# Kernel tuning notes

Hardware: AMD Instinct MI355X
Metric: run time of the kernel (lower is better)

## Reference

```python
import jax, jax.numpy as jnp
import numpy as np
import math

E, H, O, D, HD, NH, NQ, TIN = 1152, 1280, 2432, 4, 64, 20, 64, 320
FF = 4 * H
B, N = 32, 577


def _ln(x, g, b, eps=1e-5):
    m = jnp.mean(x, axis=-1, keepdims=True)
    v = jnp.var(x, axis=-1, keepdims=True)
    return (x - m) * jax.lax.rsqrt(v + eps) * g + b


def _time_proj(t):
    # get_timestep_embedding, flip_sin_to_cos=True, freq_shift=0 -> [cos, sin]
    half = TIN // 2
    freqs = jnp.exp(-math.log(10000.0) * jnp.arange(half, dtype=jnp.float32) / half)
    ang = t[:, None] * freqs[None, :]
    return jnp.concatenate([jnp.cos(ang), jnp.sin(ang)], axis=-1)


def setup_inputs() -> dict:
    key = jax.random.key(0)
    ks = iter(jax.random.split(key, 64))
    def w(shape, s=0.02):
        return jax.random.normal(next(ks), shape, jnp.float32) * s
    return {
        "x": jax.random.normal(next(ks), (B, N, E), jnp.float32),
        "timestep": jax.random.uniform(next(ks), (B,), jnp.float32) * 1000.0,
        "latents0": jax.random.normal(next(ks), (1, NQ, H), jnp.float32) / math.sqrt(H),
        "proj_in_W": w((E, H)), "proj_in_b": jnp.zeros((H,), jnp.float32),
        "te1_W": w((TIN, H)), "te1_b": jnp.zeros((H,), jnp.float32),
        "te2_W": w((H, H)), "te2_b": jnp.zeros((H,), jnp.float32),
        "ln0_g": jnp.ones((D, H), jnp.float32), "ln0_b": jnp.zeros((D, H), jnp.float32),
        "ln1_g": jnp.ones((D, H), jnp.float32), "ln1_b": jnp.zeros((D, H), jnp.float32),
        "Wq": w((D, H, H)), "Wkv": w((D, H, 2 * H)), "Wo": w((D, H, H)),
        "ada_W": w((D, H, 4 * H)), "ada_b": jnp.zeros((D, 4 * H), jnp.float32),
        "lnada_g": jnp.ones((D, H), jnp.float32), "lnada_b": jnp.zeros((D, H), jnp.float32),
        "Wff1": w((D, H, FF)), "Wff2": w((D, FF, H)),
        "proj_out_W": w((H, O)), "proj_out_b": jnp.zeros((O,), jnp.float32),
        "norm_out_g": jnp.ones((O,), jnp.float32), "norm_out_b": jnp.zeros((O,), jnp.float32),
    }


def _forward(x, timestep, latents0, proj_in_W, proj_in_b, te1_W, te1_b, te2_W, te2_b,
             ln0_g, ln0_b, ln1_g, ln1_b, Wq, Wkv, Wo, ada_W, ada_b, lnada_g, lnada_b,
             Wff1, Wff2, proj_out_W, proj_out_b, norm_out_g, norm_out_b):
    b = x.shape[0]
    t_emb = _time_proj(timestep)
    t_emb = jax.nn.silu(t_emb @ te1_W + te1_b) @ te2_W + te2_b  # [B,H]
    h = x @ proj_in_W + proj_in_b + t_emb[:, None]              # [B,N,H]
    lat = jnp.broadcast_to(latents0, (b, NQ, H))
    s = 1.0 / math.sqrt(math.sqrt(HD))
    for i in range(D):
        emb = jax.nn.silu(t_emb) @ ada_W[i] + ada_b[i]
        sh_msa, sc_msa, sh_mlp, sc_mlp = jnp.split(emb, 4, axis=1)
        res = lat
        xn = _ln(h, ln0_g[i], ln0_b[i])
        lm = _ln(lat, ln1_g[i], ln1_b[i]) * (1.0 + sc_msa[:, None]) + sh_msa[:, None]
        q = (lm @ Wq[i]).reshape(b, NQ, NH, HD).transpose(0, 2, 1, 3)
        kv = jnp.concatenate([xn, lm], axis=1) @ Wkv[i]         # [B,N+NQ,2H]
        k, v = jnp.split(kv, 2, axis=-1)
        nk = k.shape[1]
        k = k.reshape(b, nk, NH, HD).transpose(0, 2, 1, 3)
        v = v.reshape(b, nk, NH, HD).transpose(0, 2, 1, 3)
        wts = jnp.einsum('bhqd,bhkd->bhqk', q * s, k * s)
        wts = jax.nn.softmax(wts.astype(jnp.float32), axis=-1).astype(q.dtype)
        att = jnp.einsum('bhqk,bhkd->bhqd', wts, v).transpose(0, 2, 1, 3).reshape(b, NQ, H)
        lat = att @ Wo[i] + res
        res = lat
        lm2 = _ln(lat, lnada_g[i], lnada_b[i]) * (1.0 + sc_mlp[:, None]) + sh_mlp[:, None]
        lat = jax.nn.gelu(lm2 @ Wff1[i], approximate=False) @ Wff2[i] + res
    out = _ln(lat @ proj_out_W + proj_out_b, norm_out_g, norm_out_b)
    return out, t_emb


def reference(x, timestep, latents0, proj_in_W, proj_in_b, te1_W, te1_b, te2_W, te2_b,
              ln0_g, ln0_b, ln1_g, ln1_b, Wq, Wkv, Wo, ada_W, ada_b, lnada_g, lnada_b,
              Wff1, Wff2, proj_out_W, proj_out_b, norm_out_g, norm_out_b):
    return _forward(x, timestep, latents0, proj_in_W, proj_in_b, te1_W, te1_b, te2_W,
                    te2_b, ln0_g, ln0_b, ln1_g, ln1_b, Wq, Wkv, Wo, ada_W, ada_b,
                    lnada_g, lnada_b, Wff1, Wff2, proj_out_W, proj_out_b, norm_out_g,
                    norm_out_b)
```

## Files before the change

kernel.cpp:

```cpp
#include <hip/hip_runtime.h>
#include <cstdint>
#include <cstddef>

typedef unsigned short u16;
typedef unsigned int u32;
typedef __bf16 bf16x8 __attribute__((ext_vector_type(8)));
typedef float f32x4 __attribute__((ext_vector_type(4)));

__device__ inline float bf2f(u16 h){ union{u32 u; float f;} v; v.u = ((u32)h)<<16; return v.f; }
__device__ inline u16 f2bf(float f){ union{float f; u32 u;} v; v.f=f; u32 r = v.u + 0x7fffu + ((v.u>>16)&1u); return (u16)(r>>16); }

union V16 { uint4 u; bf16x8 b; };

__device__ inline void gll16(const u16* g, u16* l){
  __builtin_amdgcn_global_load_lds(
      (const __attribute__((address_space(1))) u32*)g,
      (__attribute__((address_space(3))) u32*)l,
      16, 0, 0);
}

__device__ inline float2 block_red_sum2(float a, float b){
  #pragma unroll
  for (int o=32;o;o>>=1){ a += __shfl_xor(a,o,64); b += __shfl_xor(b,o,64); }
  __shared__ float ta[4], tb[4];
  int w = threadIdx.x>>6;
  if ((threadIdx.x&63)==0){ ta[w]=a; tb[w]=b; }
  __syncthreads();
  float ra = ta[0]+ta[1]+ta[2]+ta[3];
  float rb = tb[0]+tb[1]+tb[2]+tb[3];
  __syncthreads();
  return make_float2(ra, rb);
}

__global__ __launch_bounds__(256) void kw_gemm(
    const u16* __restrict__ A, const u16* __restrict__ B, void* __restrict__ C,
    int M, int Nclamp, int Nout, int K, int lda, int ldb, int ldc,
    long long sA1, long long sA2, long long sB1, long long sB2, long long sC1, long long sC2,
    int zdiv, int flags,
    const float* __restrict__ bias, const float* __restrict__ temb, int rowdiv,
    const float* __restrict__ res, int ldres)
{
  int z = blockIdx.z;
  int z1 = z / zdiv, z2 = z - z1*zdiv;
  A += z1*sA1 + z2*sA2;
  B += z1*sB1 + z2*sB2;
  long long coff = z1*sC1 + z2*sC2;

  __shared__ u16 As[2*128*32];
  __shared__ u16 Bs[2*128*32];

  int tid  = threadIdx.x;
  int lane = tid & 63, wave = tid >> 6;
  int wm = (wave >> 1) * 64, wn = (wave & 1) * 64;
  int lr = lane & 15, quad = lane >> 4;

  int rowBase = blockIdx.y * 128;
  int colBase = blockIdx.x * 128;

  int srow = wave*16 + (lane >> 2);
  int sseg = ((lane & 3) ^ ((lane >> 3) & 3)) * 8;

  int ar0 = min(rowBase + srow, M-1);
  int ar1 = min(rowBase + 64 + srow, M-1);
  int br0 = min(colBase + srow, Nclamp-1);
  int br1 = min(colBase + 64 + srow, Nclamp-1);
  const u16* ap0 = A + (long long)ar0*lda + sseg;
  const u16* ap1 = A + (long long)ar1*lda + sseg;
  const u16* bp0 = B + (long long)br0*ldb + sseg;
  const u16* bp1 = B + (long long)br1*ldb + sseg;

  u16* lA0 = As + wave*512;
  u16* lA1 = As + 2048 + wave*512;
  u16* lB0 = Bs + wave*512;
  u16* lB1 = Bs + 2048 + wave*512;

  int swz = (lr >> 1) & 3;
  int rdA = lr*32 + ((quad ^ swz) * 8);

  f32x4 acc[4][4];
  #pragma unroll
  for (int mi=0; mi<4; mi++)
    #pragma unroll
    for (int ni=0; ni<4; ni++) acc[mi][ni] = (f32x4){0.f,0.f,0.f,0.f};

  int wmb = wm >> 4;
  int wnb = wn >> 4;

  for (int k0 = 0; k0 < K; k0 += 64) {
    gll16(ap0, lA0);
    gll16(ap1, lA1);
    gll16(bp0, lB0);
    gll16(bp1, lB1);
    gll16(ap0+32, lA0+4096);
    gll16(ap1+32, lA1+4096);
    gll16(bp0+32, lB0+4096);
    gll16(bp1+32, lB1+4096);
    __syncthreads();

    {
      V16 af[4], bf[4];
      #pragma unroll
      for (int mi=0; mi<4; mi++) af[mi].u = *(const uint4*)&As[(wmb + mi)*512 + rdA];
      #pragma unroll
      for (int ni=0; ni<4; ni++) bf[ni].u = *(const uint4*)&Bs[(wnb + ni)*512 + rdA];
      #pragma unroll
      for (int mi=0; mi<4; mi++)
        #pragma unroll
        for (int ni=0; ni<4; ni++)
          acc[mi][ni] = __builtin_amdgcn_mfma_f32_16x16x32_bf16(af[mi].b, bf[ni].b, acc[mi][ni], 0, 0, 0);
    }
    {
      V16 af[4], bf[4];
      #pragma unroll
      for (int mi=0; mi<4; mi++) af[mi].u = *(const uint4*)&As[4096 + (wmb + mi)*512 + rdA];
      #pragma unroll
      for (int ni=0; ni<4; ni++) bf[ni].u = *(const uint4*)&Bs[4096 + (wnb + ni)*512 + rdA];
      #pragma unroll
      for (int mi=0; mi<4; mi++)
        #pragma unroll
        for (int ni=0; ni<4; ni++)
          acc[mi][ni] = __builtin_amdgcn_mfma_f32_16x16x32_bf16(af[mi].b, bf[ni].b, acc[mi][ni], 0, 0, 0);
    }

    __syncthreads();
    ap0 += 64; ap1 += 64; bp0 += 64; bp1 += 64;
  }

  #pragma unroll
  for (int mi=0; mi<4; mi++){
    #pragma unroll
    for (int ni=0; ni<4; ni++){
      #pragma unroll
      for (int rr=0; rr<4; rr++){
        int row = rowBase + wm + mi*16 + quad*4 + rr;
        int col = colBase + wn + ni*16 + lr;
        if (row < M && col < Nout){
          float x = acc[mi][ni][rr];
          if (flags & 1) x += bias[col];
          if (flags & 2) x += temb[(long long)(row/rowdiv)*1280 + col];
          if (flags & 4) x += res[(long long)row*ldres + col];
          if (flags & 8) x = 0.5f*x*(1.f + erff(x*0.70710678118654752f));
          long long o = coff + (long long)row*ldc + col;
          if (flags & 16) ((u16*)C)[o] = f2bf(x);
          else            ((float*)C)[o] = x;
        }
      }
    }
  }
}

__global__ __launch_bounds__(256) void kw_flash(
    const u16* __restrict__ qb, const u16* __restrict__ kvb,
    const u16* __restrict__ Vt, u16* __restrict__ att)
{
  int z = blockIdx.x;
  int b = z / 20, h = z - b*20;
  int tid = threadIdx.x, lane = tid & 63, wave = tid >> 6;
  int lr = lane & 15, quad = lane >> 4;

  __shared__ u16 P[4][16][72];

  const u16* qrow = qb + ((long long)(b*64 + wave*16 + lr))*1280 + h*64;
  V16 aq[2];
  aq[0].u = *(const uint4*)(qrow + quad*8);
  aq[1].u = *(const uint4*)(qrow + 32 + quad*8);

  f32x4 Oacc[4];
  #pragma unroll
  for (int nt=0; nt<4; nt++) Oacc[nt] = (f32x4){0.f,0.f,0.f,0.f};
  float mst[4], lst[4];
  #pragma unroll
  for (int rr=0; rr<4; rr++){ mst[rr] = -3e38f; lst[rr] = 0.f; }

  const u16* kbase = kvb + (long long)b*641*2560 + h*64;
  const u16* vtb   = Vt + (long long)z*64*672;

  for (int kt = 0; kt < 11; kt++){
    int key0 = kt*64;
    V16 bk0[4], bk1[4];
    #pragma unroll
    for (int nt=0; nt<4; nt++){
      int key = min(key0 + nt*16 + lr, 640);
      const u16* kr = kbase + (long long)key*2560;
      bk0[nt].u = *(const uint4*)(kr + quad*8);
      bk1[nt].u = *(const uint4*)(kr + 32 + quad*8);
    }
    f32x4 S[4];
    #pragma unroll
    for (int nt=0; nt<4; nt++){
      S[nt] = (f32x4){0.f,0.f,0.f,0.f};
      S[nt] = __builtin_amdgcn_mfma_f32_16x16x32_bf16(aq[0].b, bk0[nt].b, S[nt], 0,0,0);
      S[nt] = __builtin_amdgcn_mfma_f32_16x16x32_bf16(aq[1].b, bk1[nt].b, S[nt], 0,0,0);
    }
    float rm[4];
    #pragma unroll
    for (int rr=0; rr<4; rr++) rm[rr] = -3e38f;
    #pragma unroll
    for (int nt=0; nt<4; nt++){
      bool valid = (key0 + nt*16 + lr) < 641;
      #pragma unroll
      for (int rr=0; rr<4; rr++){
        float v = valid ? S[nt][rr]*0.125f : -3e38f;
        S[nt][rr] = v;
        rm[rr] = fmaxf(rm[rr], v);
      }
    }
    #pragma unroll
    for (int o=1; o<16; o<<=1)
      #pragma unroll
      for (int rr=0; rr<4; rr++) rm[rr] = fmaxf(rm[rr], __shfl_xor(rm[rr], o, 64));
    float alpha[4];
    #pragma unroll
    for (int rr=0; rr<4; rr++){
      float mn = fmaxf(mst[rr], rm[rr]);
      alpha[rr] = __expf(mst[rr] - mn);
      mst[rr] = mn;
    }
    float rs[4] = {0.f,0.f,0.f,0.f};
    #pragma unroll
    for (int nt=0; nt<4; nt++)
      #pragma unroll
      for (int rr=0; rr<4; rr++){
        float p = __expf(S[nt][rr] - mst[rr]);
        S[nt][rr] = p;
        rs[rr] += p;
      }
    #pragma unroll
    for (int o=1; o<16; o<<=1)
      #pragma unroll
      for (int rr=0; rr<4; rr++) rs[rr] += __shfl_xor(rs[rr], o, 64);
    #pragma unroll
    for (int rr=0; rr<4; rr++) lst[rr] = lst[rr]*alpha[rr] + rs[rr];
    #pragma unroll
    for (int nt=0; nt<4; nt++)
      #pragma unroll
      for (int rr=0; rr<4; rr++)
        P[wave][quad*4+rr][nt*16+lr] = f2bf(S[nt][rr]);
    __syncthreads();
    #pragma unroll
    for (int nt=0; nt<4; nt++)
      #pragma unroll
      for (int rr=0; rr<4; rr++) Oacc[nt][rr] *= alpha[rr];
    V16 ap[2];
    ap[0].u = *(const uint4*)&P[wave][lr][quad*8];
    ap[1].u = *(const uint4*)&P[wave][lr][32 + quad*8];
    #pragma unroll
    for (int nt=0; nt<4; nt++){
      const u16* vr = vtb + (long long)(nt*16 + lr)*672 + key0;
      V16 bv0, bv1;
      bv0.u = *(const uint4*)(vr + quad*8);
      bv1.u = *(const uint4*)(vr + 32 + quad*8);
      Oacc[nt] = __builtin_amdgcn_mfma_f32_16x16x32_bf16(ap[0].b, bv0.b, Oacc[nt], 0,0,0);
      Oacc[nt] = __builtin_amdgcn_mfma_f32_16x16x32_bf16(ap[1].b, bv1.b, Oacc[nt], 0,0,0);
    }
    __syncthreads();
  }
  float inv[4];
  #pragma unroll
  for (int rr=0; rr<4; rr++) inv[rr] = 1.0f / lst[rr];
  #pragma unroll
  for (int nt=0; nt<4; nt++)
    #pragma unroll
    for (int rr=0; rr<4; rr++){
      long long row = b*64 + wave*16 + quad*4 + rr;
      att[row*1280 + h*64 + nt*16 + lr] = f2bf(Oacc[nt][rr]*inv[rr]);
    }
}

__global__ __launch_bounds__(256) void kw_transpose(const float* __restrict__ in, u16* __restrict__ out,
                                                    int K, int N)
{
  __shared__ u16 t[64][68];
  int k0 = blockIdx.x*64, n0 = blockIdx.y*64;
  int tid = threadIdx.x; int c = tid & 63; int r4 = tid >> 6;
  #pragma unroll
  for (int p = 0; p < 16; p++){
    int kr = r4 + p*4;
    t[kr][c] = f2bf(in[(long long)(k0+kr)*N + n0 + c]);
  }
  __syncthreads();
  #pragma unroll
  for (int p = 0; p < 16; p++){
    int nr = r4 + p*4;
    out[(long long)(n0+nr)*K + k0 + c] = t[c][nr];
  }
}

__global__ __launch_bounds__(256) void kw_vt(const u16* __restrict__ kv, u16* __restrict__ Vt)
{
  int z = blockIdx.x; int kt = blockIdx.y;
  int b = z / 20, hh = z - b*20;
  const u16* src = kv + (long long)b*641*2560 + 1280 + hh*64;
  u16* dst = Vt + (long long)z*64*672;
  __shared__ u16 t[64][68];
  int tid = threadIdx.x; int c = tid & 63; int r4 = tid >> 6;
  #pragma unroll
  for (int p = 0; p < 16; p++){
    int krow = r4 + p*4;
    int key = kt*64 + krow;
    t[krow][c] = (key < 641) ? src[(long long)key*2560 + c] : (u16)0;
  }
  __syncthreads();
  #pragma unroll
  for (int p = 0; p < 16; p++){
    int d = r4 + p*4;
    int key = kt*64 + c;
    if (key < 672) dst[(long long)d*672 + key] = t[c][d];
  }
}

__global__ void kw_timeproj(const float* __restrict__ tstep, float* __restrict__ tproj)
{
  int b = blockIdx.x; int j = threadIdx.x;
  float t = tstep[b];
  int idx = (j < 160) ? j : (j - 160);
  float freq = expf(-9.210340371976184f * (float)idx / 160.0f);
  float a = t * freq;
  tproj[b*320 + j] = (j < 160) ? cosf(a) : sinf(a);
}

__global__ void kw_bias_bcast(const float* __restrict__ bias, float* __restrict__ out, int N)
{
  int b = blockIdx.x; int n = blockIdx.y*256 + threadIdx.x;
  if (n < N) out[(long long)b*N + n] = bias[n];
}

__global__ __launch_bounds__(256) void kw_mlp2(const float* __restrict__ in, const float* __restrict__ W,
    float* __restrict__ out, int K, int N, int kc)
{
  int n = blockIdx.x*256 + threadIdx.x;
  int k0 = blockIdx.y * kc;
  __shared__ float sbuf[32*160];
  for (int idx = threadIdx.x; idx < 32*kc; idx += 256){
    int b = idx / kc, k = idx - b*kc;
    sbuf[idx] = in[(long long)b*K + k0 + k];
  }
  __syncthreads();
  float acc[32];
  #pragma unroll
  for (int b=0;b<32;b++) acc[b]=0.f;
  const float* wp = W + (long long)k0*N + n;
  for (int k=0;k<kc;k++){
    float wv = wp[(long long)k*N];
    #pragma unroll
    for (int b=0;b<32;b++) acc[b] = fmaf(sbuf[b*kc+k], wv, acc[b]);
  }
  #pragma unroll
  for (int b=0;b<32;b++) atomicAdd(out + (long long)b*N + n, acc[b]);
}

__global__ void kw_silu_ip(float* __restrict__ p, int n)
{
  int i = blockIdx.x*256 + threadIdx.x;
  if (i < n){ float x = p[i]; p[i] = x/(1.f+expf(-x)); }
}

__global__ void kw_post_temb(const float* __restrict__ temb, float* __restrict__ silu_t,
                             float* __restrict__ tout, int n)
{
  int i = blockIdx.x*256 + threadIdx.x;
  if (i < n){
    float x = temb[i];
    silu_t[i] = x/(1.f+expf(-x));
    tout[i] = x;
  }
}

__global__ void kw_ada_init(const float* __restrict__ ada_b, float* __restrict__ ada)
{
  int idx = blockIdx.x*256 + threadIdx.x;
  if (idx < 4*32*5120){
    int i = idx / (32*5120);
    int j = idx % 5120;
    ada[idx] = ada_b[i*5120 + j];
  }
}

__global__ __launch_bounds__(256) void kw_ada(const float* __restrict__ silu_t,
    const float* __restrict__ adaW, float* __restrict__ ada)
{
  int jt = blockIdx.x, i = blockIdx.y, ks = blockIdx.z;
  int tid = threadIdx.x;
  int j = jt*256 + tid;
  __shared__ float sbuf[32][160];
  #pragma unroll
  for (int p = 0; p < 20; p++){
    int idx = tid + p*256;
    int b = idx / 160, k = idx - b*160;
    sbuf[b][k] = silu_t[b*1280 + ks*160 + k];
  }
  __syncthreads();
  float acc[32];
  #pragma unroll
  for (int b=0;b<32;b++) acc[b]=0.f;
  const float* wp = adaW + ((long long)i*1280 + ks*160)*5120 + j;
  for (int k=0;k<160;k++){
    float w = wp[(long long)k*5120];
    #pragma unroll
    for (int b=0;b<32;b++) acc[b] = fmaf(sbuf[b][k], w, acc[b]);
  }
  float* op = ada + (long long)i*32*5120 + j;
  for (int b=0;b<32;b++) atomicAdd(op + (long long)b*5120, acc[b]);
}

__global__ void kw_init_lat(const float* __restrict__ l0, float* __restrict__ lat)
{
  int r = blockIdx.x; int q = r & 63;
  #pragma unroll
  for (int i=0;i<5;i++){
    int c = threadIdx.x + i*256;
    lat[(long long)r*1280 + c] = l0[q*1280 + c];
  }
}

__global__ void kw_cvt(const float* __restrict__ in, u16* __restrict__ out, long long n4)
{
  long long i = ((long long)blockIdx.x*256 + threadIdx.x);
  if (i < n4){
    float4 v = *(const float4*)(in + i*4);
    u32 lo = (u32)f2bf(v.x) | ((u32)f2bf(v.y)<<16);
    u32 hi = (u32)f2bf(v.z) | ((u32)f2bf(v.w)<<16);
    uint2 o; o.x = lo; o.y = hi;
    *(uint2*)(out + i*4) = o;
  }
}

__global__ __launch_bounds__(256) void kw_ln_x(const u16* __restrict__ h, u16* __restrict__ cat,
    const float* __restrict__ g, const float* __restrict__ bb)
{
  int r = blockIdx.x;
  int batch = r / 577; int rr = r - batch*577;
  const u16* row = h + (long long)r*1280;
  u16* orow = cat + ((long long)batch*641 + rr)*1280;
  int tid = threadIdx.x;
  float v[5]; float s=0.f, s2=0.f;
  #pragma unroll
  for (int i=0;i<5;i++){ float x = bf2f(row[tid+i*256]); v[i]=x; s+=x; s2+=x*x; }
  float2 r2 = block_red_sum2(s, s2);
  float mean = r2.x * (1.f/1280.f);
  float var  = r2.y * (1.f/1280.f) - mean*mean;
  float rstd = rsqrtf(var + 1e-5f);
  #pragma unroll
  for (int i=0;i<5;i++){
    int c = tid+i*256;
    orow[c] = f2bf((v[i]-mean)*rstd*g[c] + bb[c]);
  }
}

__global__ __launch_bounds__(256) void kw_ln_mod(const float* __restrict__ lat, u16* __restrict__ out1,
    u16* __restrict__ cat, const float* __restrict__ g, const float* __restrict__ bb,
    const float* __restrict__ adabase)
{
  int r = blockIdx.x;
  int b = r >> 6, q = r & 63;
  const float* row = lat + (long long)r*1280;
  const float* ab = adabase + (long long)b*5120;
  int tid = threadIdx.x;
  float v[5]; float s=0.f, s2=0.f;
  #pragma unroll
  for (int i=0;i<5;i++){ float x = row[tid+i*256]; v[i]=x; s+=x; s2+=x*x; }
  float2 r2 = block_red_sum2(s, s2);
  float mean = r2.x * (1.f/1280.f);
  float var  = r2.y * (1.f/1280.f) - mean*mean;
  float rstd = rsqrtf(var + 1e-5f);
  #pragma unroll
  for (int i=0;i<5;i++){
    int c = tid+i*256;
    float sh = ab[c], sc = ab[1280+c];
    float y = ((v[i]-mean)*rstd*g[c] + bb[c])*(1.f+sc) + sh;
    u16 o = f2bf(y);
    out1[(long long)r*1280 + c] = o;
    if (cat) cat[((long long)b*641 + 577 + q)*1280 + c] = o;
  }
}

__global__ __launch_bounds__(256) void kw_ln_out(const float* __restrict__ in, float* __restrict__ out,
    const float* __restrict__ g, const float* __restrict__ bb)
{
  int r = blockIdx.x;
  const float* row = in + (long long)r*2432;
  int tid = threadIdx.x;
  float v[10]; float s=0.f, s2=0.f;
  #pragma unroll
  for (int i=0;i<10;i++){
    int c = tid + i*256;
    float x = (c < 2432) ? row[c] : 0.f;
    v[i]=x; s+=x; s2+=x*x;
  }
  float2 r2 = block_red_sum2(s, s2);
  float mean = r2.x * (1.f/2432.f);
  float var  = r2.y * (1.f/2432.f) - mean*mean;
  float rstd = rsqrtf(var + 1e-5f);
  #pragma unroll
  for (int i=0;i<10;i++){
    int c = tid + i*256;
    if (c < 2432) out[(long long)r*2432 + c] = (v[i]-mean)*rstd*g[c] + bb[c];
  }
}

static inline void launch_gemm(hipStream_t s, const u16* A, const u16* B, void* C,
    int M, int Nclamp, int Nout, int K, int lda, int ldb, int ldc,
    int nz, int zdiv, long long sA1, long long sA2, long long sB1, long long sB2,
    long long sC1, long long sC2, int flags,
    const float* bias = nullptr, const float* temb = nullptr, int rowdiv = 1,
    const float* res = nullptr, int ldres = 0)
{
  dim3 g((Nout+127)/128, (M+127)/128, nz);
  kw_gemm<<<g, dim3(256), 0, s>>>(A,B,C,M,Nclamp,Nout,K,lda,ldb,ldc,
      sA1,sA2,sB1,sB2,sC1,sC2,zdiv,flags,bias,temb,rowdiv,res,ldres);
}

extern "C" void kernel_launch(void* const* d_in, const int* in_sizes, int n_in,
                              void* d_out, int out_size, void* d_ws, size_t ws_size,
                              hipStream_t stream)
{
  const float* x         = (const float*)d_in[0];
  const float* timestep  = (const float*)d_in[1];
  const float* latents0  = (const float*)d_in[2];
  const float* proj_in_W = (const float*)d_in[3];
  const float* proj_in_b = (const float*)d_in[4];
  const float* te1_W     = (const float*)d_in[5];
  const float* te1_b     = (const float*)d_in[6];
  const float* te2_W     = (const float*)d_in[7];
  const float* te2_b     = (const float*)d_in[8];
  const float* ln0_g     = (const float*)d_in[9];
  const float* ln0_b     = (const float*)d_in[10];
  const float* ln1_g     = (const float*)d_in[11];
  const float* ln1_b     = (const float*)d_in[12];
  const float* Wq        = (const float*)d_in[13];
  const float* Wkv       = (const float*)d_in[14];
  const float* Wo        = (const float*)d_in[15];
  const float* ada_W     = (const float*)d_in[16];
  const float* ada_b     = (const float*)d_in[17];
  const float* lnada_g   = (const float*)d_in[18];
  const float* lnada_b   = (const float*)d_in[19];
  const float* Wff1      = (const float*)d_in[20];
  const float* Wff2      = (const float*)d_in[21];
  const float* proj_out_W= (const float*)d_in[22];
  const float* proj_out_b= (const float*)d_in[23];
  const float* norm_out_g= (const float*)d_in[24];
  const float* norm_out_b= (const float*)d_in[25];
  float* out = (float*)d_out;

  const long long MX = 18464;
  const long long MC = 20512;

  char* w = (char*)d_ws; size_t off = 0;
  auto alloc = [&](size_t bytes)->void*{ void* p = w + off; off += (bytes + 255) & ~(size_t)255; return p; };

  float* tproj  = (float*)alloc(32*320*4);
  float* hidden = (float*)alloc(32*1280*4);
  float* temb   = (float*)alloc(32*1280*4);
  float* silu_t = (float*)alloc(32*1280*4);
  float* ada    = (float*)alloc(4*32*5120*4);
  u16*  h    = (u16*)alloc(MX*1280*2);
  u16*  cat  = (u16*)alloc(MC*1280*2);
  u16*  lm   = (u16*)alloc(2048*1280*2);
  u16*  lm2  = (u16*)alloc(2048*1280*2);
  u16*  qb   = (u16*)alloc(2048*1280*2);
  u16*  att  = (u16*)alloc(2048*1280*2);
  float* lat = (float*)alloc(2048*1280*4);
  u16*  kvb  = (u16*)alloc(MC*2560*2);
  u16*  Vt   = (u16*)alloc((long long)640*64*672*2);
  u16*  WT_pi  = (u16*)alloc(1280*1152*2);
  u16*  WT_po  = (u16*)alloc((long long)2432*1280*2);
  u16*  WqT    = (u16*)alloc(1280*1280*2);
  u16*  WkvT   = (u16*)alloc(2560*1280*2);
  u16*  WoT    = (u16*)alloc(1280*1280*2);
  u16*  Wff1T  = (u16*)alloc((long long)5120*1280*2);
  u16*  Wff2T  = (u16*)alloc((long long)1280*5120*2);
  char* R = (char*)alloc((long long)2048*5120*2 + 4096);
  u16*  xbf    = (u16*)R;
  u16*  ffh    = (u16*)R;
  float* po    = (float*)R;

  if (off > ws_size) return;

  kw_timeproj<<<dim3(32), dim3(320), 0, stream>>>(timestep, tproj);
  kw_bias_bcast<<<dim3(32,5), dim3(256), 0, stream>>>(te1_b, hidden, 1280);
  kw_mlp2<<<dim3(5,4), dim3(256), 0, stream>>>(tproj, te1_W, hidden, 320, 1280, 80);
  kw_silu_ip<<<dim3(160), dim3(256), 0, stream>>>(hidden, 32*1280);
  kw_bias_bcast<<<dim3(32,5), dim3(256), 0, stream>>>(te2_b, temb, 1280);
  kw_mlp2<<<dim3(5,8), dim3(256), 0, stream>>>(hidden, te2_W, temb, 1280, 1280, 160);
  kw_post_temb<<<dim3(160), dim3(256), 0, stream>>>(temb, silu_t, out + (long long)2048*2432, 32*1280);

  kw_ada_init<<<dim3(2560), dim3(256), 0, stream>>>(ada_b, ada);
  kw_ada<<<dim3(20,4,8), dim3(256), 0, stream>>>(silu_t, ada_W, ada);

  kw_cvt<<<dim3((unsigned)((MX*1152/4 + 255)/256)), dim3(256), 0, stream>>>(x, xbf, MX*1152/4);
  kw_transpose<<<dim3(18,20), dim3(256), 0, stream>>>(proj_in_W, WT_pi, 1152, 1280);
  launch_gemm(stream, xbf, WT_pi, h, (int)MX, 1280, 1280, 1152, 1152, 1152, 1280,
              1, 1, 0,0,0,0,0,0, 1|2|16, proj_in_b, temb, 577);

  kw_init_lat<<<dim3(2048), dim3(256), 0, stream>>>(latents0, lat);
  kw_transpose<<<dim3(20,38), dim3(256), 0, stream>>>(proj_out_W, WT_po, 1280, 2432);

  for (int i = 0; i < 4; i++){
    kw_transpose<<<dim3(20,20), dim3(256), 0, stream>>>(Wq   + (long long)i*1280*1280, WqT,   1280, 1280);
    kw_transpose<<<dim3(20,40), dim3(256), 0, stream>>>(Wkv  + (long long)i*1280*2560, WkvT,  1280, 2560);
    kw_transpose<<<dim3(20,20), dim3(256), 0, stream>>>(Wo   + (long long)i*1280*1280, WoT,   1280, 1280);
    kw_transpose<<<dim3(20,80), dim3(256), 0, stream>>>(Wff1 + (long long)i*1280*5120, Wff1T, 1280, 5120);
    kw_transpose<<<dim3(80,20), dim3(256), 0, stream>>>(Wff2 + (long long)i*5120*1280, Wff2T, 5120, 1280);

    kw_ln_x<<<dim3((unsigned)MX), dim3(256), 0, stream>>>(h, cat, ln0_g + i*1280, ln0_b + i*1280);
    kw_ln_mod<<<dim3(2048), dim3(256), 0, stream>>>(lat, lm, cat, ln1_g + i*1280, ln1_b + i*1280,
                                                    ada + (long long)i*32*5120 + 0);
    launch_gemm(stream, lm,  WqT,  qb,  2048, 1280, 1280, 1280, 1280, 1280, 1280, 1, 1, 0,0,0,0,0,0, 16);
    launch_gemm(stream, cat, WkvT, kvb, (int)MC, 2560, 2560, 1280, 1280, 1280, 2560, 1, 1, 0,0,0,0,0,0, 16);
    kw_vt<<<dim3(640,11), dim3(256), 0, stream>>>(kvb, Vt);
    kw_flash<<<dim3(640), dim3(256), 0, stream>>>(qb, kvb, Vt, att);
    launch_gemm(stream, att, WoT, lat, 2048, 1280, 1280, 1280, 1280, 1280, 1280,
                1, 1, 0,0,0,0,0,0, 4, nullptr, nullptr, 1, lat, 1280);
    kw_ln_mod<<<dim3(2048), dim3(256), 0, stream>>>(lat, lm2, nullptr, lnada_g + i*1280, lnada_b + i*1280,
                                                    ada + (long long)i*32*5120 + 2560);
    launch_gemm(stream, lm2, Wff1T, ffh, 2048, 5120, 5120, 1280, 1280, 1280, 5120,
                1, 1, 0,0,0,0,0,0, 8|16);
    launch_gemm(stream, ffh, Wff2T, lat, 2048, 1280, 1280, 5120, 5120, 5120, 1280,
                1, 1, 0,0,0,0,0,0, 4, nullptr, nullptr, 1, lat, 1280);
  }

  kw_cvt<<<dim3(2560), dim3(256), 0, stream>>>(lat, lm, 2048*1280/4);
  launch_gemm(stream, lm, WT_po, po, 2048, 2432, 2432, 1280, 1280, 1280, 2432,
              1, 1, 0,0,0,0,0,0, 1, proj_out_b);
  kw_ln_out<<<dim3(2048), dim3(256), 0, stream>>>(po, out, norm_out_g, norm_out_b);
}
```

Measured before the change: 3.610 ms.

## Add 256x256-tile pipelined GEMM kernel for large projections

Adds a 512-thread GEMM with 256x256 output tiles, 128 KB of dynamic LDS, double-buffered direct global-to-LDS loads, swizzled LDS layout, XCD-aware workgroup remapping and setprio around MFMA bursts. It replaces the 128x128 GEMM for the proj_in, KV and FF1 GEMMs, aiming to raise data reuse per tile and overlap loads with MFMA work. The main loop steps K in chunks of 128 without handling remainders. Proj_in has K=1152, which is 9 chunks, and the other two use K=1280, so all divide evenly. Larger tiles give fewer workgroups and more waste on edge tiles, for example MX=18464 rows.

New measurement: 3.941 ms. 1.09x slower.

```diff
diff --git a/kernel.cpp b/kernel.cpp
--- a/kernel.cpp
+++ b/kernel.cpp
@@ -149,6 +149,142 @@
   }
 }
 
+__global__ __launch_bounds__(512, 2) void kw_gemm256(
+    const u16* __restrict__ A, const u16* __restrict__ B, void* __restrict__ C,
+    int M, int Nclamp, int Nout, int K, int lda, int ldb, int ldc, int flags,
+    const float* __restrict__ bias, const float* __restrict__ temb, int rowdiv,
+    const float* __restrict__ res, int ldres)
+{
+  extern __shared__ u16 lds[];
+
+  int tid = threadIdx.x;
+  int lane = tid & 63, wave = tid >> 6;
+  int wm = wave >> 2, wn = wave & 3;
+  int lr = lane & 15, quad = lane >> 4;
+  int l8 = lane >> 3;
+  int ksw = ((lane & 7) ^ l8) << 3;
+
+  int gx = gridDim.x, gy = gridDim.y;
+  int nwg = gx * gy;
+  int orig = blockIdx.y * gx + blockIdx.x;
+  int qq = nwg >> 3, rmn = nwg & 7;
+  int xcd = orig & 7, loc = orig >> 3;
+  int wgid = (xcd < rmn ? xcd * (qq + 1) : rmn * (qq + 1) + (xcd - rmn) * qq) + loc;
+  int bx = wgid % gx, by = wgid / gx;
+
+  int rowBase = by * 256, colBase = bx * 256;
+
+  const u16* aS[2][2]; const u16* bS[2][2];
+  #pragma unroll
+  for (int g=0; g<2; g++){
+    #pragma unroll
+    for (int r=0; r<2; r++){
+      int grow = rowBase + g*64 + r*128 + wave*8 + l8;
+      grow = min(grow, M-1);
+      aS[g][r] = A + (long long)grow*lda + ksw;
+      int gcol = colBase + (r*2 + wm)*64 + g*32 + wn*8 + l8;
+      gcol = min(gcol, Nclamp-1);
+      bS[g][r] = B + (long long)gcol*ldb + ksw;
+    }
+  }
+
+  u16* A00 = lds;          u16* A01 = lds + 8192;
+  u16* A10 = lds + 16384;  u16* A11 = lds + 24576;
+  u16* B00 = lds + 32768;  u16* B01 = lds + 40960;
+  u16* B10 = lds + 49152;  u16* B11 = lds + 57344;
+
+  int dA0 = wave*512, dA1 = 4096 + wave*512;
+
+  int rdA = (wm*64 + lr)*64;
+  int rdB = (wn*32 + lr)*64;
+  int ksw2 = (lr & 7) << 3;
+  int k0off = (quad*8) ^ ksw2;
+  int k1off = (32 + quad*8) ^ ksw2;
+
+  f32x4 acc[8][4];
+  #pragma unroll
+  for (int i=0;i<8;i++)
+    #pragma unroll
+    for (int j=0;j<4;j++) acc[i][j] = (f32x4){0.f,0.f,0.f,0.f};
+
+#define STG(SRC, G, REG, KO) do{ gll16(SRC[G][0]+(KO), (REG)+dA0); gll16(SRC[G][1]+(KO), (REG)+dA1); }while(0)
+#define RD_AF(REG) do{ _Pragma("unroll") for (int m2=0;m2<4;m2++){ \
+    af[m2][0].u = *(const uint4*)((REG) + rdA + m2*1024 + k0off); \
+    af[m2][1].u = *(const uint4*)((REG) + rdA + m2*1024 + k1off); } }while(0)
+#define RD_BF(NB, REG) do{ _Pragma("unroll") for (int n2=0;n2<2;n2++){ \
+    bf[(NB)+n2][0].u = *(const uint4*)((REG) + rdB + n2*1024 + k0off); \
+    bf[(NB)+n2][1].u = *(const uint4*)((REG) + rdB + n2*1024 + k1off); } }while(0)
+#define MM8(MI, NI) do{ _Pragma("unroll") for (int m2=0;m2<4;m2++) \
+    _Pragma("unroll") for (int n2=0;n2<2;n2++){ \
+      acc[(MI)+m2][(NI)+n2] = __builtin_amdgcn_mfma_f32_16x16x32_bf16(af[m2][0].b, bf[(NI)+n2][0].b, acc[(MI)+m2][(NI)+n2],0,0,0); \
+      acc[(MI)+m2][(NI)+n2] = __builtin_amdgcn_mfma_f32_16x16x32_bf16(af[m2][1].b, bf[(NI)+n2][1].b, acc[(MI)+m2][(NI)+n2],0,0,0); } }while(0)
+#define BARRIER() asm volatile("s_barrier" ::: "memory")
+#define VMCNT6()  asm volatile("s_waitcnt vmcnt(6)" ::: "memory")
+
+  STG(aS,0,A00,0); STG(bS,0,B00,0); STG(bS,1,B01,0); STG(aS,1,A01,0);
+  STG(aS,0,A10,64); STG(bS,0,B10,64); STG(bS,1,B11,64);
+  VMCNT6();
+  BARRIER();
+
+  int nIt = K >> 7;
+  for (int it = 0; it < nIt; ++it){
+    int kA1 = (it<<7) + 64;
+    int kN0 = (it<<7) + 128; if (kN0 >= K) kN0 = 0;
+    int kN1 = (it<<7) + 192; if (kN1 >= K) kN1 = 0;
+
+    V16 af[4][2], bf[4][2];
+
+    RD_AF(A00); RD_BF(0, B00); STG(aS,1,A11,kA1);
+    BARRIER(); __builtin_amdgcn_s_setprio(1); MM8(0,0); __builtin_amdgcn_s_setprio(0); BARRIER();
+    RD_BF(2, B01); STG(aS,0,A00,kN0);
+    BARRIER(); __builtin_amdgcn_s_setprio(1); MM8(0,2); __builtin_amdgcn_s_setprio(0); BARRIER();
+    RD_AF(A01); STG(bS,0,B00,kN0);
+    BARRIER(); __builtin_amdgcn_s_setprio(1); MM8(4,2); __builtin_amdgcn_s_setprio(0); BARRIER();
+    STG(bS,1,B01,kN0);
+    BARRIER(); __builtin_amdgcn_s_setprio(1); MM8(4,0); __builtin_amdgcn_s_setprio(0);
+    VMCNT6(); BARRIER();
+    RD_AF(A10); RD_BF(0, B10); STG(aS,1,A01,kN0);
+    BARRIER(); __builtin_amdgcn_s_setprio(1); MM8(0,0); __builtin_amdgcn_s_setprio(0); BARRIER();
+    RD_BF(2, B11); STG(aS,0,A10,kN1);
+    BARRIER(); __builtin_amdgcn_s_setprio(1); MM8(0,2); __builtin_amdgcn_s_setprio(0); BARRIER();
+    RD_AF(A11); STG(bS,0,B10,kN1);
+    BARRIER(); __builtin_amdgcn_s_setprio(1); MM8(4,2); __builtin_amdgcn_s_setprio(0); BARRIER();
+    STG(bS,1,B11,kN1);
+    BARRIER(); __builtin_amdgcn_s_setprio(1); MM8(4,0); __builtin_amdgcn_s_setprio(0);
+    VMCNT6(); BARRIER();
+  }
+
+  asm volatile("s_waitcnt vmcnt(0)" ::: "memory");
+
+  #pragma unroll
+  for (int mi=0; mi<8; mi++){
+    #pragma unroll
+    for (int ni=0; ni<4; ni++){
+      int col = colBase + wn*64 + (ni>>1)*32 + (ni&1)*16 + lr;
+      #pragma unroll
+      for (int rr=0; rr<4; rr++){
+        int row = rowBase + wm*128 + (mi>>2)*64 + (mi&3)*16 + quad*4 + rr;
+        if (row < M && col < Nout){
+          float x = acc[mi][ni][rr];
+          if (flags & 1) x += bias[col];
+          if (flags & 2) x += temb[(long long)(row/rowdiv)*1280 + col];
+          if (flags & 4) x += res[(long long)row*ldres + col];
+          if (flags & 8) x = 0.5f*x*(1.f + erff(x*0.70710678118654752f));
+          long long o = (long long)row*ldc + col;
+          if (flags & 16) ((u16*)C)[o] = f2bf(x);
+          else            ((float*)C)[o] = x;
+        }
+      }
+    }
+  }
+#undef STG
+#undef RD_AF
+#undef RD_BF
+#undef MM8
+#undef BARRIER
+#undef VMCNT6
+}
+
 __global__ __launch_bounds__(256) void kw_flash(
     const u16* __restrict__ qb, const u16* __restrict__ kvb,
     const u16* __restrict__ Vt, u16* __restrict__ att)
@@ -510,10 +646,27 @@
       sA1,sA2,sB1,sB2,sC1,sC2,zdiv,flags,bias,temb,rowdiv,res,ldres);
 }
 
+static inline void launch_gemm256(hipStream_t s, const u16* A, const u16* B, void* C,
+    int M, int Nclamp, int Nout, int K, int lda, int ldb, int ldc, int flags,
+    const float* bias = nullptr, const float* temb = nullptr, int rowdiv = 1,
+    const float* res = nullptr, int ldres = 0)
+{
+  dim3 g((Nout+255)/256, (M+255)/256, 1);
+  kw_gemm256<<<g, dim3(512), 131072, s>>>(A,B,C,M,Nclamp,Nout,K,lda,ldb,ldc,flags,
+      bias,temb,rowdiv,res,ldres);
+}
+
 extern "C" void kernel_launch(void* const* d_in, const int* in_sizes, int n_in,
                               void* d_out, int out_size, void* d_ws, size_t ws_size,
                               hipStream_t stream)
 {
+  static bool shmem_set = false;
+  if (!shmem_set){
+    hipFuncSetAttribute((const void*)kw_gemm256,
+                        hipFuncAttributeMaxDynamicSharedMemorySize, 131072);
+    shmem_set = true;
+  }
+
   const float* x         = (const float*)d_in[0];
   const float* timestep  = (const float*)d_in[1];
   const float* latents0  = (const float*)d_in[2];
@@ -589,8 +742,8 @@
 
   kw_cvt<<<dim3((unsigned)((MX*1152/4 + 255)/256)), dim3(256), 0, stream>>>(x, xbf, MX*1152/4);
   kw_transpose<<<dim3(18,20), dim3(256), 0, stream>>>(proj_in_W, WT_pi, 1152, 1280);
-  launch_gemm(stream, xbf, WT_pi, h, (int)MX, 1280, 1280, 1152, 1152, 1152, 1280,
-              1, 1, 0,0,0,0,0,0, 1|2|16, proj_in_b, temb, 577);
+  launch_gemm256(stream, xbf, WT_pi, h, (int)MX, 1280, 1280, 1152, 1152, 1152, 1280,
+                 1|2|16, proj_in_b, temb, 577);
 
   kw_init_lat<<<dim3(2048), dim3(256), 0, stream>>>(latents0, lat);
   kw_transpose<<<dim3(20,38), dim3(256), 0, stream>>>(proj_out_W, WT_po, 1280, 2432);
@@ -606,15 +759,14 @@
     kw_ln_mod<<<dim3(2048), dim3(256), 0, stream>>>(lat, lm, cat, ln1_g + i*1280, ln1_b + i*1280,
                                                     ada + (long long)i*32*5120 + 0);
     launch_gemm(stream, lm,  WqT,  qb,  2048, 1280, 1280, 1280, 1280, 1280, 1280, 1, 1, 0,0,0,0,0,0, 16);
-    launch_gemm(stream, cat, WkvT, kvb, (int)MC, 2560, 2560, 1280, 1280, 1280, 2560, 1, 1, 0,0,0,0,0,0, 16);
+    launch_gemm256(stream, cat, WkvT, kvb, (int)MC, 2560, 2560, 1280, 1280, 1280, 2560, 16);
     kw_vt<<<dim3(640,11), dim3(256), 0, stream>>>(kvb, Vt);
     kw_flash<<<dim3(640), dim3(256), 0, stream>>>(qb, kvb, Vt, att);
     launch_gemm(stream, att, WoT, lat, 2048, 1280, 1280, 1280, 1280, 1280, 1280,
                 1, 1, 0,0,0,0,0,0, 4, nullptr, nullptr, 1, lat, 1280);
     kw_ln_mod<<<dim3(2048), dim3(256), 0, stream>>>(lat, lm2, nullptr, lnada_g + i*1280, lnada_b + i*1280,
                                                     ada + (long long)i*32*5120 + 2560);
-    launch_gemm(stream, lm2, Wff1T, ffh, 2048, 5120, 5120, 1280, 1280, 1280, 5120,
-                1, 1, 0,0,0,0,0,0, 8|16);
+    launch_gemm256(stream, lm2, Wff1T, ffh, 2048, 5120, 5120, 1280, 1280, 1280, 5120, 8|16);
     launch_gemm(stream, ffh, Wff2T, lat, 2048, 1280, 1280, 5120, 5120, 5120, 1280,
                 1, 1, 0,0,0,0,0,0, 4, nullptr, nullptr, 1, lat, 1280);
   }
```
